# Performance work log

Hardware: AMD Instinct MI355X
Metric: run time of the kernel (lower is better)

Reference implementation:

```python
import jax, jax.numpy as jnp
import numpy as np

# Scalars from init_kwargs (qat_training=False inference path)
IN_ZP = 0
OUT_ZP = 0
IN_SCALE = 0.02
OUT_SCALE = 0.05
STRIDE = (1, 1)
PAD = (1, 1)      # (ph, pw); module pads (pw, pw, ph, ph) via F.pad
DIL = (1, 1)
GROUPS = 1
QMIN, QMAX = -128, 127  # get_quantized_range(8)


def setup_inputs() -> dict:
    key = jax.random.key(0)
    k1, k2, k3, k4 = jax.random.split(key, 4)
    x = jax.random.randint(k1, (32, 128, 56, 56), -128, 128, dtype=jnp.int32).astype(jnp.int8)
    weight = jax.random.randint(k2, (256, 128, 3, 3), -128, 128, dtype=jnp.int32).astype(jnp.int8)
    bias = jax.random.randint(k3, (256,), -1000, 1000, dtype=jnp.int32)
    weight_scale = jax.random.uniform(k4, (256,), minval=1e-3, maxval=1e-2, dtype=jnp.float32)
    return {"x": x, "weight": weight, "bias": bias, "weight_scale": weight_scale}


def reference(x, weight, bias, weight_scale):
    # Pad spatial dims with the input zero point (matches F.pad(..., value=input_zero_point))
    xp = jnp.pad(x.astype(jnp.int32),
                 ((0, 0), (0, 0), (PAD[0], PAD[0]), (PAD[1], PAD[1])),
                 constant_values=IN_ZP)
    # Exact int32-accumulate convolution (torch CPU path)
    acc = jax.lax.conv_general_dilated(
        xp, weight.astype(jnp.int32),
        window_strides=STRIDE, padding='VALID', rhs_dilation=DIL,
        dimension_numbers=('NCHW', 'OIHW', 'NCHW'),
        feature_group_count=GROUPS, preferred_element_type=jnp.int32)
    acc = acc + bias[None, :, None, None]
    # Per-output-channel requantization
    scale = (IN_SCALE * weight_scale / OUT_SCALE)[None, :, None, None]
    out = acc.astype(jnp.float32) * scale + OUT_ZP
    out = jnp.clip(jnp.round(out), QMIN, QMAX).astype(jnp.int8)
    return out
```

## Files before the change

### kernel.cpp

```cpp
#include <hip/hip_runtime.h>
#include <hip/hip_bf16.h>
#include <stdint.h>


#define NB   32
#define CIN  128
#define HO   56
#define WO   56
#define KOUT 256
#define HP   58
#define ROWB (HP * CIN)

typedef int v4i  __attribute__((ext_vector_type(4)));
typedef int v16i __attribute__((ext_vector_type(16)));

static __device__ __forceinline__ void gload_lds16(const int8_t* g, int8_t* l) {
  __builtin_amdgcn_global_load_lds(
      (const __attribute__((address_space(1))) void*)g,
      (__attribute__((address_space(3))) void*)l, 16, 0, 0);
}

__global__ __launch_bounds__(256) void pack_x_kernel(const int* __restrict__ x,
                                                     int8_t* __restrict__ xp) {
  __shared__ int t32[128][57];
  const int tid = threadIdx.x;
  const int r = blockIdx.x;
  const int n = blockIdx.y;
  const bool interior = (r >= 1) && (r <= HO);

  if (interior) {
    const int h = r - 1;
    const int* xrow = x + ((size_t)(n * CIN) * HO + h) * WO;
    #pragma unroll
    for (int it = 0; it < 7; ++it) {
      const int j = it * 256 + tid;
      const int c = j / 14;
      const int w4 = j - c * 14;
      const int4 v = *reinterpret_cast<const int4*>(xrow + c * 3136 + w4 * 4);
      t32[c][w4 * 4 + 0] = v.x;
      t32[c][w4 * 4 + 1] = v.y;
      t32[c][w4 * 4 + 2] = v.z;
      t32[c][w4 * 4 + 3] = v.w;
    }
  }
  __syncthreads();
  #pragma unroll
  for (int it = 0; it < 8; ++it) {
    const int i = it * 256 + tid;
    if (i < HP * 32) {
      const int wi = i & 3;
      const int w = (i >> 2) % HP;
      const int cc = (i >> 2) / HP;
      const int c4 = cc * 4 + wi;
      int vv = 0;
      if (interior && w >= 1 && w <= WO) {
        const int b0 = t32[c4 * 4 + 0][w - 1] & 0xff;
        const int b1 = t32[c4 * 4 + 1][w - 1] & 0xff;
        const int b2 = t32[c4 * 4 + 2][w - 1] & 0xff;
        const int b3 = t32[c4 * 4 + 3][w - 1];
        vv = b0 | (b1 << 8) | (b2 << 16) | (b3 << 24);
      }
      *reinterpret_cast<int*>(
          xp + ((size_t)(n * HP + r) * 8 + cc) * 928 + w * 16 + wi * 4) = vv;
    }
  }
}

__global__ __launch_bounds__(256) void pack_w_kernel(const int* __restrict__ wgt,
                                                     int8_t* __restrict__ wq) {
  const int wid = blockIdx.x * 256 + threadIdx.x;
  const int wi = wid & 3;
  const int ci = wid >> 2;
  const int kt = ci / 4608;
  const int r  = ci - kt * 4608;
  const int tap = r >> 9;
  const int r2  = r & 511;
  const int cc  = r2 >> 6;
  const int ch  = r2 & 63;
  const int k_global = kt * 64 + ch;
  const int cin0 = cc * 16 + wi * 4;
  const int base = (k_global * CIN + cin0) * 9 + tap;
  const int v0 = wgt[base];
  const int v1 = wgt[base + 9];
  const int v2 = wgt[base + 18];
  const int v3 = wgt[base + 27];
  reinterpret_cast<int*>(wq)[wid] =
      (v0 & 0xff) | ((v1 & 0xff) << 8) | ((v2 & 0xff) << 16) | (v3 << 24);
}

__global__ __launch_bounds__(512, 4) void conv_kernel(const int8_t* __restrict__ xp,
                                                      const int8_t* __restrict__ wq,
                                                      const int* __restrict__ bias,
                                                      const float* __restrict__ wscale,
                                                      int* __restrict__ out) {
  __shared__ __align__(16) int8_t lw[9 * 8 * 64 * 16];
  __shared__ int   bsh[64];
  __shared__ float ssh[64];

  const int tid = threadIdx.x;
  const int rg = blockIdx.x;
  const int n_img = blockIdx.y;
  const int kt = blockIdx.z;
  const int h0 = rg * 8;

  const int lane = tid & 63;
  const int wr = tid >> 6;
  const int p0 = lane & 31;
  const int half = lane >> 5;

  const int8_t* wqt = wq + (size_t)kt * 73728;
  #pragma unroll
  for (int it = 0; it < 9; ++it) {
    const int j = it * 512 + tid;
    gload_lds16(wqt + j * 16, lw + j * 16);
  }
  if (tid < 64) {
    const int ch = kt * 64 + tid;
    bsh[tid] = bias[ch];
    ssh[tid] = (0.02f * wscale[ch]) / 0.05f;
  }
  __syncthreads();

  v16i acc[2][2];
  #pragma unroll
  for (int mt = 0; mt < 2; ++mt)
    #pragma unroll
    for (int nt = 0; nt < 2; ++nt)
      #pragma unroll
      for (int e = 0; e < 16; ++e) acc[mt][nt][e] = 0;

  const int8_t* xb = xp + ((size_t)(n_img * HP + h0 + wr) * 8) * 928 + p0 * 16;

  #pragma unroll 1
  for (int tap = 0; tap < 9; ++tap) {
    const int kh = (tap >= 3) + (tap >= 6);
    const int kw = tap - 3 * kh;
    const int8_t* lwt = lw + tap * 8192;
    const int8_t* xrow = xb + (kh * 8) * 928 + kw * 16;
    #pragma unroll
    for (int ks = 0; ks < 4; ++ks) {
      const int cch = 2 * ks + half;
      const v4i a0 = *reinterpret_cast<const v4i*>(lwt + cch * 1024 + p0 * 16);
      const v4i a1 = *reinterpret_cast<const v4i*>(lwt + cch * 1024 + p0 * 16 + 512);
      const v4i b0 = *reinterpret_cast<const v4i*>(xrow + cch * 928);
      const v4i b1 = *reinterpret_cast<const v4i*>(xrow + cch * 928 + 512);
      acc[0][0] = __builtin_amdgcn_mfma_i32_32x32x32_i8(a0, b0, acc[0][0], 0, 0, 0);
      acc[1][0] = __builtin_amdgcn_mfma_i32_32x32x32_i8(a1, b0, acc[1][0], 0, 0, 0);
      acc[0][1] = __builtin_amdgcn_mfma_i32_32x32x32_i8(a0, b1, acc[0][1], 0, 0, 0);
      acc[1][1] = __builtin_amdgcn_mfma_i32_32x32x32_i8(a1, b1, acc[1][1], 0, 0, 0);
    }
  }

  const int h = h0 + wr;
  #pragma unroll
  for (int mt = 0; mt < 2; ++mt) {
    #pragma unroll
    for (int r = 0; r < 16; ++r) {
      const int cl = mt * 32 + (r & 3) + 8 * (r >> 2) + 4 * half;
      const int bi = bsh[cl];
      const float sc = ssh[cl];
      int* ob = out + (((size_t)(n_img * KOUT + kt * 64 + cl)) * HO + h) * WO;
      #pragma unroll
      for (int nt = 0; nt < 2; ++nt) {
        const int w = nt * 32 + p0;
        if (w < WO) {
          float v = (float)(acc[mt][nt][r] + bi) * sc;
          v = rintf(v);
          v = fminf(fmaxf(v, -128.0f), 127.0f);
          ob[w] = (int)v;
        }
      }
    }
  }
}

extern "C" void kernel_launch(void* const* d_in, const int* in_sizes, int n_in,
                              void* d_out, int out_size, void* d_ws, size_t ws_size,
                              hipStream_t stream) {
  const int* x = (const int*)d_in[0];
  const int* wgt = (const int*)d_in[1];
  const int* bias = (const int*)d_in[2];
  const float* wscale = (const float*)d_in[3];
  int* out = (int*)d_out;

  int8_t* xp = (int8_t*)d_ws;
  int8_t* wq = (int8_t*)d_ws + (size_t)NB * HP * ROWB;

  pack_x_kernel<<<dim3(HP, NB), 256, 0, stream>>>(x, xp);
  pack_w_kernel<<<288, 256, 0, stream>>>(wgt, wq);
  conv_kernel<<<dim3(7, 32, 4), 512, 0, stream>>>(xp, wq, bias, wscale, out);
}
```

Measured before the change: 189.2 us.

## Stage input rows in LDS with XOR swizzle, read weights from global

Swaps which operand is held in LDS. Each block now stages four padded input rows (NHWC layout with a swizzled channel-chunk order) into shared memory, and streams the weight fragments straight from global/L2. Blocks shrink to 256 threads covering two output rows, with four times as many blocks, and each wave owns a 32-channel slice with two accumulators. The pack kernel writes a plain NHWC layout to match. This cuts the 72KB per-block weight preload and raises occupancy, at the cost of repeated global weight loads inside the MFMA loop.

Measured after the change: 186.3 us. No clear change (-1.5%).

```diff
diff --git a/kernel.cpp b/kernel.cpp
--- a/kernel.cpp
+++ b/kernel.cpp
@@ -48,10 +48,8 @@
   for (int it = 0; it < 8; ++it) {
     const int i = it * 256 + tid;
     if (i < HP * 32) {
-      const int wi = i & 3;
-      const int w = (i >> 2) % HP;
-      const int cc = (i >> 2) / HP;
-      const int c4 = cc * 4 + wi;
+      const int w = i >> 5;
+      const int c4 = i & 31;
       int vv = 0;
       if (interior && w >= 1 && w <= WO) {
         const int b0 = t32[c4 * 4 + 0][w - 1] & 0xff;
@@ -60,8 +58,7 @@
         const int b3 = t32[c4 * 4 + 3][w - 1];
         vv = b0 | (b1 << 8) | (b2 << 16) | (b3 << 24);
       }
-      *reinterpret_cast<int*>(
-          xp + ((size_t)(n * HP + r) * 8 + cc) * 928 + w * 16 + wi * 4) = vv;
+      *reinterpret_cast<int*>(xp + ((size_t)(n * HP + r) * HP + w) * CIN + c4 * 4) = vv;
     }
   }
 }
@@ -88,12 +85,12 @@
       (v0 & 0xff) | ((v1 & 0xff) << 8) | ((v2 & 0xff) << 16) | (v3 << 24);
 }
 
-__global__ __launch_bounds__(512, 4) void conv_kernel(const int8_t* __restrict__ xp,
+__global__ __launch_bounds__(256, 4) void conv_kernel(const int8_t* __restrict__ xp,
                                                       const int8_t* __restrict__ wq,
                                                       const int* __restrict__ bias,
                                                       const float* __restrict__ wscale,
                                                       int* __restrict__ out) {
-  __shared__ __align__(16) int8_t lw[9 * 8 * 64 * 16];
+  __shared__ __align__(16) int8_t lx[(4 * HP + 8) * 8 * 16];
   __shared__ int   bsh[64];
   __shared__ float ssh[64];
 
@@ -101,18 +98,26 @@
   const int rg = blockIdx.x;
   const int n_img = blockIdx.y;
   const int kt = blockIdx.z;
-  const int h0 = rg * 8;
+  const int h0 = rg * 2;
 
   const int lane = tid & 63;
-  const int wr = tid >> 6;
+  const int wv = tid >> 6;
+  const int wr = wv & 1;
+  const int slice = wv >> 1;
   const int p0 = lane & 31;
   const int half = lane >> 5;
 
-  const int8_t* wqt = wq + (size_t)kt * 73728;
+  const int8_t* xg = xp + ((size_t)(n_img * HP) + h0) * ROWB;
+  const int8_t* wqt = wq + (size_t)kt * 73728 + (slice * 32 + p0) * 16;
+
   #pragma unroll
-  for (int it = 0; it < 9; ++it) {
-    const int j = it * 512 + tid;
-    gload_lds16(wqt + j * 16, lw + j * 16);
+  for (int it = 0; it < 8; ++it) {
+    const int i = it * 256 + tid;
+    if (i < 4 * HP * 8) {
+      const int pf = i >> 3;
+      const int cc = (i & 7) ^ (pf & 7);
+      gload_lds16(xg + pf * CIN + (cc << 4), lx + i * 16);
+    }
   }
   if (tid < 64) {
     const int ch = kt * 64 + tid;
@@ -121,54 +126,45 @@
   }
   __syncthreads();
 
-  v16i acc[2][2];
+  v16i acc[2];
   #pragma unroll
-  for (int mt = 0; mt < 2; ++mt)
+  for (int nt = 0; nt < 2; ++nt)
     #pragma unroll
-    for (int nt = 0; nt < 2; ++nt)
-      #pragma unroll
-      for (int e = 0; e < 16; ++e) acc[mt][nt][e] = 0;
+    for (int e = 0; e < 16; ++e) acc[nt][e] = 0;
 
-  const int8_t* xb = xp + ((size_t)(n_img * HP + h0 + wr) * 8) * 928 + p0 * 16;
-
-  #pragma unroll 1
+  #pragma unroll
   for (int tap = 0; tap < 9; ++tap) {
     const int kh = (tap >= 3) + (tap >= 6);
     const int kw = tap - 3 * kh;
-    const int8_t* lwt = lw + tap * 8192;
-    const int8_t* xrow = xb + (kh * 8) * 928 + kw * 16;
+    const int pfb = (wr + kh) * HP + kw;
     #pragma unroll
     for (int ks = 0; ks < 4; ++ks) {
       const int cch = 2 * ks + half;
-      const v4i a0 = *reinterpret_cast<const v4i*>(lwt + cch * 1024 + p0 * 16);
-      const v4i a1 = *reinterpret_cast<const v4i*>(lwt + cch * 1024 + p0 * 16 + 512);
-      const v4i b0 = *reinterpret_cast<const v4i*>(xrow + cch * 928);
-      const v4i b1 = *reinterpret_cast<const v4i*>(xrow + cch * 928 + 512);
-      acc[0][0] = __builtin_amdgcn_mfma_i32_32x32x32_i8(a0, b0, acc[0][0], 0, 0, 0);
-      acc[1][0] = __builtin_amdgcn_mfma_i32_32x32x32_i8(a1, b0, acc[1][0], 0, 0, 0);
-      acc[0][1] = __builtin_amdgcn_mfma_i32_32x32x32_i8(a0, b1, acc[0][1], 0, 0, 0);
-      acc[1][1] = __builtin_amdgcn_mfma_i32_32x32x32_i8(a1, b1, acc[1][1], 0, 0, 0);
+      const v4i a = *reinterpret_cast<const v4i*>(wqt + tap * 8192 + cch * 1024);
+      const int pf0 = pfb + p0;
+      const int pf1 = pfb + 32 + p0;
+      const v4i b0 = *reinterpret_cast<const v4i*>(lx + pf0 * CIN + ((cch ^ (pf0 & 7)) << 4));
+      const v4i b1 = *reinterpret_cast<const v4i*>(lx + pf1 * CIN + ((cch ^ (pf1 & 7)) << 4));
+      acc[0] = __builtin_amdgcn_mfma_i32_32x32x32_i8(a, b0, acc[0], 0, 0, 0);
+      acc[1] = __builtin_amdgcn_mfma_i32_32x32x32_i8(a, b1, acc[1], 0, 0, 0);
     }
   }
 
   const int h = h0 + wr;
   #pragma unroll
-  for (int mt = 0; mt < 2; ++mt) {
+  for (int r = 0; r < 16; ++r) {
+    const int cl = slice * 32 + (r & 3) + 8 * (r >> 2) + 4 * half;
+    const int bi = bsh[cl];
+    const float sc = ssh[cl];
+    int* ob = out + (((size_t)(n_img * KOUT + kt * 64 + cl)) * HO + h) * WO;
     #pragma unroll
-    for (int r = 0; r < 16; ++r) {
-      const int cl = mt * 32 + (r & 3) + 8 * (r >> 2) + 4 * half;
-      const int bi = bsh[cl];
-      const float sc = ssh[cl];
-      int* ob = out + (((size_t)(n_img * KOUT + kt * 64 + cl)) * HO + h) * WO;
-      #pragma unroll
-      for (int nt = 0; nt < 2; ++nt) {
-        const int w = nt * 32 + p0;
-        if (w < WO) {
-          float v = (float)(acc[mt][nt][r] + bi) * sc;
-          v = rintf(v);
-          v = fminf(fmaxf(v, -128.0f), 127.0f);
-          ob[w] = (int)v;
-        }
+    for (int nt = 0; nt < 2; ++nt) {
+      const int w = nt * 32 + p0;
+      if (w < WO) {
+        float v = (float)(acc[nt][r] + bi) * sc;
+        v = rintf(v);
+        v = fminf(fmaxf(v, -128.0f), 127.0f);
+        ob[w] = (int)v;
       }
     }
   }
@@ -188,5 +184,5 @@
 
   pack_x_kernel<<<dim3(HP, NB), 256, 0, stream>>>(x, xp);
   pack_w_kernel<<<288, 256, 0, stream>>>(wgt, wq);
-  conv_kernel<<<dim3(7, 32, 4), 512, 0, stream>>>(xp, wq, bias, wscale, out);
+  conv_kernel<<<dim3(28, 32, 4), 256, 0, stream>>>(xp, wq, bias, wscale, out);
 }
```
